# Kernel tuning notes

Measured on AMD Instinct MI355X. Metric: run time of the kernel, lower is better.

The kernel has to match this reference:

```python
import jax, jax.numpy as jnp
import numpy as np

Q_MAX = 127.0  # int8 activation quant range
NIB_MASK = 15  # 4-bit mask


def setup_inputs() -> dict:
    key = jax.random.key(0)
    k1, k2, k3, k4, k5 = jax.random.split(key, 5)
    M, IN, OUT = 4096, 4096, 11008
    x = jax.random.normal(k1, (M, IN), dtype=jnp.float32)
    # packed int4 weights: two nibbles per byte, [OUT, IN//2]
    qweight = jax.random.randint(k2, (OUT, IN // 2), 0, 256, dtype=jnp.int32)
    qzeros = jax.random.randint(k3, (OUT, 1), 0, 16, dtype=jnp.int32)
    scales = jax.random.uniform(k4, (OUT, 1), dtype=jnp.float32) * 0.01 + 1e-4
    bias = jax.random.normal(k5, (OUT,), dtype=jnp.float32) * 0.01
    clampv = jnp.full((1,), 3.0, dtype=jnp.float32)
    return {"x": x, "qweight": qweight, "qzeros": qzeros,
            "scales": scales, "bias": bias, "clampv": clampv}


def _unpack_int4(qweight, qzeros, scales):
    # high nibble -> even position, low nibble -> odd position (matches torch unpack)
    hi = (qweight >> 4) & NIB_MASK          # [OUT, IN//2]
    lo = qweight & NIB_MASK                 # [OUT, IN//2]
    intw = jnp.stack([hi, lo], axis=-1).reshape(qweight.shape[0], -1)  # [OUT, IN]
    return (intw - qzeros).astype(scales.dtype) * scales               # [OUT, IN]


def reference(x, qweight, qzeros, scales, bias, clampv):
    cv = clampv[0]
    # static activation fake-quant at scale clampv/127 (quantize_activation_static)
    x = jnp.clip(x, -cv, cv)
    a_scale = cv / Q_MAX
    qx = jnp.clip(jnp.round(x / a_scale), -Q_MAX, Q_MAX) * a_scale
    # dequantize packed int4 weights, then GEMM
    W = _unpack_int4(qweight, qzeros, scales)   # [OUT, IN]
    out = qx @ W.T + bias[None, :]              # [M, OUT]
    return out
```

## Files before the change

kernel.cpp:

```cpp
#include <hip/hip_runtime.h>
#include <stdint.h>

typedef int v4i __attribute__((ext_vector_type(4)));

static constexpr int Mdim = 4096;
static constexpr int Kdim = 4096;
static constexpr int Ndim = 11008;

#define BM 256
#define BN 256
#define BK 128
#define NT (Kdim / BK)

__device__ __forceinline__ void gload_lds16(const void* gp, void* lp) {
  __builtin_amdgcn_global_load_lds((const __attribute__((address_space(1))) void*)gp,
                                   (__attribute__((address_space(3))) void*)lp,
                                   16, 0, 0);
}

__global__ void k_quant(const float* __restrict__ x, const float* __restrict__ clampv,
                        signed char* __restrict__ qa, int* __restrict__ rowsum) {
  const int row = blockIdx.x;
  const int t = threadIdx.x;
  const float cv = clampv[0];
  const float a_scale = cv / 127.0f;
  const float4* xp = (const float4*)(x + (size_t)row * Kdim) + t * 4;
  int s = 0;
  int w[4];
#pragma unroll
  for (int i = 0; i < 4; ++i) {
    float4 f = xp[i];
    float q0 = fminf(fmaxf(rintf(fminf(fmaxf(f.x, -cv), cv) / a_scale), -127.f), 127.f);
    float q1 = fminf(fmaxf(rintf(fminf(fmaxf(f.y, -cv), cv) / a_scale), -127.f), 127.f);
    float q2 = fminf(fmaxf(rintf(fminf(fmaxf(f.z, -cv), cv) / a_scale), -127.f), 127.f);
    float q3 = fminf(fmaxf(rintf(fminf(fmaxf(f.w, -cv), cv) / a_scale), -127.f), 127.f);
    int i0 = (int)q0, i1 = (int)q1, i2 = (int)q2, i3 = (int)q3;
    s += i0 + i1 + i2 + i3;
    w[i] = (i0 & 255) | ((i1 & 255) << 8) | ((i2 & 255) << 16) | ((i3 & 255) << 24);
  }
  ((int4*)(qa + (size_t)row * Kdim))[t] = make_int4(w[0], w[1], w[2], w[3]);
#pragma unroll
  for (int off = 32; off > 0; off >>= 1) s += __shfl_down(s, off, 64);
  __shared__ int red[4];
  if ((t & 63) == 0) red[t >> 6] = s;
  __syncthreads();
  if (t == 0) rowsum[row] = red[0] + red[1] + red[2] + red[3];
}

__global__ void k_unpack(const int4* __restrict__ qw, uint2* __restrict__ wb) {
  const int idx = blockIdx.x * 256 + threadIdx.x;
  int4 q = qw[idx];
  uint2 r;
  r.x = (unsigned)(((q.x >> 4) & 15) | ((q.x & 15) << 8) |
                   (((q.y >> 4) & 15) << 16) | ((q.y & 15) << 24));
  r.y = (unsigned)(((q.z >> 4) & 15) | ((q.z & 15) << 8) |
                   (((q.w >> 4) & 15) << 16) | ((q.w & 15) << 24));
  wb[idx] = r;
}

__global__ __launch_bounds__(512, 2) void k_gemm(
    const signed char* __restrict__ A, const signed char* __restrict__ B,
    const float* __restrict__ scales, const int* __restrict__ qzeros,
    const float* __restrict__ bias, const float* __restrict__ clampv,
    const int* __restrict__ rowsum, float* __restrict__ out) {
  __shared__ signed char lds[131072];
  signed char* As = lds;
  signed char* Bs = lds + 65536;

  const int t = threadIdx.x;
  const int lane = t & 63;
  const int wave = t >> 6;
  const int wm = (wave >> 2) * 128;
  const int wn = (wave & 3) * 64;

  const int bid = blockIdx.x;
  const int swz = (bid & 7) * 86 + (bid >> 3);
  const int mt = swz / 43;
  const int nt = swz - mt * 43;
  const int m0 = mt * BM;
  const int n0 = nt * BN;

  const int srow = t >> 3;
  const int sch = (t & 7) ^ (srow & 7);
  const signed char* gA = A + (size_t)(m0 + srow) * Kdim + sch * 16;
  const signed char* gB = B + (size_t)(n0 + srow) * Kdim + sch * 16;
  const int sdst = t * 16;

#define STAGE_A(buf, k0)                                               \
  {                                                                    \
    _Pragma("unroll") for (int i = 0; i < 4; ++i)                      \
        gload_lds16(gA + (size_t)(i * 64) * Kdim + (k0),               \
                    As + (buf) * 32768 + i * 8192 + sdst);             \
  }
#define STAGE_B(buf, k0)                                               \
  {                                                                    \
    _Pragma("unroll") for (int i = 0; i < 4; ++i)                      \
        gload_lds16(gB + (size_t)(i * 64) * Kdim + (k0),               \
                    Bs + (buf) * 32768 + i * 8192 + sdst);             \
  }

  const int col = lane & 15;
  const int q16 = lane >> 4;
  const int c7 = col & 7;
  int aoff[2], boff[2];
#pragma unroll
  for (int ks = 0; ks < 2; ++ks) {
    const int pos = ((ks * 4 + q16) ^ c7) * 16;
    aoff[ks] = (wm + col) * BK + pos;
    boff[ks] = (wn + col) * BK + pos;
  }

  v4i acc[8][4] = {};
  v4i a[4][2], b[4][2];

  STAGE_A(0, 0);
  STAGE_B(0, 0);
  asm volatile("s_waitcnt vmcnt(0)" ::: "memory");
  __builtin_amdgcn_s_barrier();

  int cur = 0;
  for (int ti = 0; ti < NT; ++ti) {
    const int nk = (ti + 1) * BK;
    const bool pf = (ti + 1 < NT);
    const signed char* Ac = As + cur * 32768;
    const signed char* Bc = Bs + cur * 32768;

    if (pf) STAGE_A(cur ^ 1, nk);
#pragma unroll
    for (int ks = 0; ks < 2; ++ks) {
#pragma unroll
      for (int i = 0; i < 4; ++i) a[i][ks] = *(const v4i*)(Ac + i * 2048 + aoff[ks]);
#pragma unroll
      for (int j = 0; j < 4; ++j) b[j][ks] = *(const v4i*)(Bc + j * 2048 + boff[ks]);
    }
    __builtin_amdgcn_s_barrier();
    __builtin_amdgcn_s_setprio(1);
#pragma unroll
    for (int ks = 0; ks < 2; ++ks)
#pragma unroll
      for (int i = 0; i < 4; ++i)
#pragma unroll
        for (int j = 0; j < 2; ++j)
          acc[i][j] = __builtin_amdgcn_mfma_i32_16x16x64_i8(a[i][ks], b[j][ks], acc[i][j], 0, 0, 0);
    __builtin_amdgcn_s_setprio(0);
    __builtin_amdgcn_s_barrier();

    if (pf) STAGE_B(cur ^ 1, nk);
    __builtin_amdgcn_s_barrier();
    __builtin_amdgcn_s_setprio(1);
#pragma unroll
    for (int ks = 0; ks < 2; ++ks)
#pragma unroll
      for (int i = 0; i < 4; ++i)
#pragma unroll
        for (int j = 2; j < 4; ++j)
          acc[i][j] = __builtin_amdgcn_mfma_i32_16x16x64_i8(a[i][ks], b[j][ks], acc[i][j], 0, 0, 0);
    __builtin_amdgcn_s_setprio(0);
    __builtin_amdgcn_s_barrier();

#pragma unroll
    for (int ks = 0; ks < 2; ++ks)
#pragma unroll
      for (int i = 0; i < 4; ++i)
        a[i][ks] = *(const v4i*)(Ac + (i + 4) * 2048 + aoff[ks]);
    __builtin_amdgcn_s_barrier();
    __builtin_amdgcn_s_setprio(1);
#pragma unroll
    for (int ks = 0; ks < 2; ++ks)
#pragma unroll
      for (int i = 0; i < 4; ++i)
#pragma unroll
        for (int j = 2; j < 4; ++j)
          acc[i + 4][j] = __builtin_amdgcn_mfma_i32_16x16x64_i8(a[i][ks], b[j][ks], acc[i + 4][j], 0, 0, 0);
    __builtin_amdgcn_s_setprio(0);
    __builtin_amdgcn_s_barrier();

    __builtin_amdgcn_s_setprio(1);
#pragma unroll
    for (int ks = 0; ks < 2; ++ks)
#pragma unroll
      for (int i = 0; i < 4; ++i)
#pragma unroll
        for (int j = 0; j < 2; ++j)
          acc[i + 4][j] = __builtin_amdgcn_mfma_i32_16x16x64_i8(a[i][ks], b[j][ks], acc[i + 4][j], 0, 0, 0);
    __builtin_amdgcn_s_setprio(0);
    asm volatile("s_waitcnt vmcnt(0)" ::: "memory");
    __builtin_amdgcn_s_barrier();
    cur ^= 1;
  }
#undef STAGE_A
#undef STAGE_B

  const float a_scale = clampv[0] / 127.0f;
  const int rq = q16 * 4;
  int rs[8][4];
#pragma unroll
  for (int i = 0; i < 8; ++i)
#pragma unroll
    for (int r = 0; r < 4; ++r)
      rs[i][r] = rowsum[m0 + wm + i * 16 + rq + r];
#pragma unroll
  for (int j = 0; j < 4; ++j) {
    const int n = n0 + wn + j * 16 + col;
    const float sn = scales[n] * a_scale;
    const int zn = qzeros[n];
    const float bn = bias[n];
#pragma unroll
    for (int i = 0; i < 8; ++i) {
      const int mb = m0 + wm + i * 16 + rq;
#pragma unroll
      for (int r = 0; r < 4; ++r) {
        const int iv = acc[i][j][r] - zn * rs[i][r];
        out[(size_t)(mb + r) * Ndim + n] = (float)iv * sn + bn;
      }
    }
  }
}

extern "C" void kernel_launch(void* const* d_in, const int* in_sizes, int n_in,
                              void* d_out, int out_size, void* d_ws, size_t ws_size,
                              hipStream_t stream) {
  const float* x  = (const float*)d_in[0];
  const int* qw   = (const int*)d_in[1];
  const int* qz   = (const int*)d_in[2];
  const float* sc = (const float*)d_in[3];
  const float* bi = (const float*)d_in[4];
  const float* cv = (const float*)d_in[5];
  float* out = (float*)d_out;

  signed char* qa = (signed char*)d_ws;
  signed char* wb = qa + (size_t)Mdim * Kdim;
  int* rowsum = (int*)(wb + (size_t)Ndim * Kdim);

  k_quant<<<Mdim, 256, 0, stream>>>(x, cv, qa, rowsum);
  k_unpack<<<(Ndim * (Kdim / 2) / 4) / 256, 256, 0, stream>>>((const int4*)qw, (uint2*)wb);
  k_gemm<<<dim3((Mdim / BM) * (Ndim / BN)), 512, 0, stream>>>(qa, wb, sc, qz, bi, cv, rowsum, out);
}
```

Measured before the change: 467.6 us.

## Switch GEMM to 32x32x32 int8 MFMA with double-buffered K-step register loads

```diff
diff --git a/kernel.cpp b/kernel.cpp
--- a/kernel.cpp
+++ b/kernel.cpp
@@ -1,7 +1,8 @@
 #include <hip/hip_runtime.h>
 #include <stdint.h>
 
-typedef int v4i __attribute__((ext_vector_type(4)));
+typedef int v4i  __attribute__((ext_vector_type(4)));
+typedef int v16i __attribute__((ext_vector_type(16)));
 
 static constexpr int Mdim = 4096;
 static constexpr int Kdim = 4096;
@@ -99,19 +100,25 @@
                     Bs + (buf) * 32768 + i * 8192 + sdst);             \
   }
 
-  const int col = lane & 15;
-  const int q16 = lane >> 4;
-  const int c7 = col & 7;
-  int aoff[2], boff[2];
-#pragma unroll
-  for (int ks = 0; ks < 2; ++ks) {
-    const int pos = ((ks * 4 + q16) ^ c7) * 16;
-    aoff[ks] = (wm + col) * BK + pos;
-    boff[ks] = (wn + col) * BK + pos;
-  }
-
-  v4i acc[8][4] = {};
-  v4i a[4][2], b[4][2];
+  const int col32 = lane & 31;
+  const int q32 = lane >> 5;
+  const int c7 = lane & 7;
+  const int abase = (wm + col32) * BK;
+  const int bbase = (wn + col32) * BK;
+  int pos[4];
+#pragma unroll
+  for (int ks = 0; ks < 4; ++ks) pos[ks] = ((ks * 2 + q32) ^ c7) * 16;
+
+  v16i acc[4][2] = {};
+  v4i a[2][4], b[2][2];
+
+#define LOADK(bank, ks_)                                                   \
+  {                                                                        \
+    _Pragma("unroll") for (int i = 0; i < 4; ++i)                          \
+        a[bank][i] = *(const v4i*)(Ac + i * 4096 + abase + pos[ks_]);      \
+    _Pragma("unroll") for (int j = 0; j < 2; ++j)                          \
+        b[bank][j] = *(const v4i*)(Bc + j * 4096 + bbase + pos[ks_]);      \
+  }
 
   STAGE_A(0, 0);
   STAGE_B(0, 0);
@@ -125,93 +132,49 @@
     const signed char* Ac = As + cur * 32768;
     const signed char* Bc = Bs + cur * 32768;
 
-    if (pf) STAGE_A(cur ^ 1, nk);
-#pragma unroll
-    for (int ks = 0; ks < 2; ++ks) {
-#pragma unroll
-      for (int i = 0; i < 4; ++i) a[i][ks] = *(const v4i*)(Ac + i * 2048 + aoff[ks]);
-#pragma unroll
-      for (int j = 0; j < 4; ++j) b[j][ks] = *(const v4i*)(Bc + j * 2048 + boff[ks]);
+    if (pf) {
+      STAGE_A(cur ^ 1, nk);
+      STAGE_B(cur ^ 1, nk);
     }
-    __builtin_amdgcn_s_barrier();
-    __builtin_amdgcn_s_setprio(1);
-#pragma unroll
-    for (int ks = 0; ks < 2; ++ks)
+
+    LOADK(0, 0);
+#pragma unroll
+    for (int ks = 0; ks < 4; ++ks) {
+      if (ks < 3) LOADK((ks + 1) & 1, ks + 1);
+      __builtin_amdgcn_s_setprio(1);
 #pragma unroll
       for (int i = 0; i < 4; ++i)
 #pragma unroll
         for (int j = 0; j < 2; ++j)
-          acc[i][j] = __builtin_amdgcn_mfma_i32_16x16x64_i8(a[i][ks], b[j][ks], acc[i][j], 0, 0, 0);
-    __builtin_amdgcn_s_setprio(0);
-    __builtin_amdgcn_s_barrier();
-
-    if (pf) STAGE_B(cur ^ 1, nk);
-    __builtin_amdgcn_s_barrier();
-    __builtin_amdgcn_s_setprio(1);
-#pragma unroll
-    for (int ks = 0; ks < 2; ++ks)
-#pragma unroll
-      for (int i = 0; i < 4; ++i)
-#pragma unroll
-        for (int j = 2; j < 4; ++j)
-          acc[i][j] = __builtin_amdgcn_mfma_i32_16x16x64_i8(a[i][ks], b[j][ks], acc[i][j], 0, 0, 0);
-    __builtin_amdgcn_s_setprio(0);
-    __builtin_amdgcn_s_barrier();
-
-#pragma unroll
-    for (int ks = 0; ks < 2; ++ks)
-#pragma unroll
-      for (int i = 0; i < 4; ++i)
-        a[i][ks] = *(const v4i*)(Ac + (i + 4) * 2048 + aoff[ks]);
-    __builtin_amdgcn_s_barrier();
-    __builtin_amdgcn_s_setprio(1);
-#pragma unroll
-    for (int ks = 0; ks < 2; ++ks)
-#pragma unroll
-      for (int i = 0; i < 4; ++i)
-#pragma unroll
-        for (int j = 2; j < 4; ++j)
-          acc[i + 4][j] = __builtin_amdgcn_mfma_i32_16x16x64_i8(a[i][ks], b[j][ks], acc[i + 4][j], 0, 0, 0);
-    __builtin_amdgcn_s_setprio(0);
-    __builtin_amdgcn_s_barrier();
-
-    __builtin_amdgcn_s_setprio(1);
-#pragma unroll
-    for (int ks = 0; ks < 2; ++ks)
-#pragma unroll
-      for (int i = 0; i < 4; ++i)
-#pragma unroll
-        for (int j = 0; j < 2; ++j)
-          acc[i + 4][j] = __builtin_amdgcn_mfma_i32_16x16x64_i8(a[i][ks], b[j][ks], acc[i + 4][j], 0, 0, 0);
-    __builtin_amdgcn_s_setprio(0);
+          acc[i][j] = __builtin_amdgcn_mfma_i32_32x32x32_i8(a[ks & 1][i], b[ks & 1][j],
+                                                            acc[i][j], 0, 0, 0);
+      __builtin_amdgcn_s_setprio(0);
+    }
+
     asm volatile("s_waitcnt vmcnt(0)" ::: "memory");
     __builtin_amdgcn_s_barrier();
     cur ^= 1;
   }
 #undef STAGE_A
 #undef STAGE_B
+#undef LOADK
 
   const float a_scale = clampv[0] / 127.0f;
-  const int rq = q16 * 4;
-  int rs[8][4];
-#pragma unroll
-  for (int i = 0; i < 8; ++i)
-#pragma unroll
-    for (int r = 0; r < 4; ++r)
-      rs[i][r] = rowsum[m0 + wm + i * 16 + rq + r];
-#pragma unroll
-  for (int j = 0; j < 4; ++j) {
-    const int n = n0 + wn + j * 16 + col;
+#pragma unroll
+  for (int j = 0; j < 2; ++j) {
+    const int n = n0 + wn + j * 32 + col32;
     const float sn = scales[n] * a_scale;
     const int zn = qzeros[n];
     const float bn = bias[n];
 #pragma unroll
-    for (int i = 0; i < 8; ++i) {
-      const int mb = m0 + wm + i * 16 + rq;
-#pragma unroll
-      for (int r = 0; r < 4; ++r) {
-        const int iv = acc[i][j][r] - zn * rs[i][r];
-        out[(size_t)(mb + r) * Ndim + n] = (float)iv * sn + bn;
+    for (int i = 0; i < 4; ++i) {
+      const int mbase = m0 + wm + i * 32;
+#pragma unroll
+      for (int r = 0; r < 16; ++r) {
+        const int row = (r & 3) + 8 * (r >> 2) + 4 * q32;
+        const int m = mbase + row;
+        const int iv = acc[i][j][r] - zn * rowsum[m];
+        out[(size_t)m * Ndim + n] = (float)iv * sn + bn;
       }
     }
   }
```

After: 475.5 us. Within noise of the previous version (+1.7%).
